# Performance work log

Hardware: AMD Instinct MI355X
Metric: run time of the kernel (lower is better)

Reference implementation:

```python
import jax, jax.numpy as jnp
import numpy as np

H = 256      # hidden_size
NH = 4       # num_heads
HD = H // NH # head_dim
N_NODES = 2048
N_EDGES = 8192
EPS = 1e-5


def _layer_norm(x, g, b):
    mu = jnp.mean(x, axis=-1, keepdims=True)
    var = jnp.mean((x - mu) ** 2, axis=-1, keepdims=True)
    return (x - mu) * jax.lax.rsqrt(var + EPS) * g + b


def setup_inputs() -> dict:
    key = jax.random.key(0)
    ks = jax.random.split(key, 16)
    s = 1.0 / np.sqrt(H)
    inp = {
        "node_features": jax.random.normal(ks[0], (N_NODES, H), jnp.float32),
        "edge_features": jax.random.normal(ks[1], (N_EDGES, H), jnp.float32),
        "in_proj_w": jax.random.uniform(ks[2], (3 * H, H), jnp.float32, -s, s),
        "in_proj_b": jnp.zeros((3 * H,), jnp.float32),
        "out_proj_w": jax.random.uniform(ks[3], (H, H), jnp.float32, -s, s),
        "out_proj_b": jnp.zeros((H,), jnp.float32),
        "mlp_w1": jax.random.uniform(ks[4], (H, H), jnp.float32, -s, s),
        "mlp_b1": jnp.zeros((H,), jnp.float32),
        "mlp_w2": jax.random.uniform(ks[5], (H, H), jnp.float32, -s, s),
        "mlp_b2": jnp.zeros((H,), jnp.float32),
        "nu_w": jax.random.uniform(ks[6], (H, H), jnp.float32, -s, s),
        "nu_b": jnp.zeros((H,), jnp.float32),
        "ln1_g": jnp.ones((H,), jnp.float32),
        "ln1_b": jnp.zeros((H,), jnp.float32),
        "ln2_g": jnp.ones((H,), jnp.float32),
        "ln2_b": jnp.zeros((H,), jnp.float32),
        "edge_index": jax.random.randint(ks[7], (2, N_EDGES), 0, N_NODES, jnp.int32),
    }
    return inp


def reference(node_features, edge_features, in_proj_w, in_proj_b, out_proj_w, out_proj_b,
              mlp_w1, mlp_b1, mlp_w2, mlp_b2, nu_w, nu_b,
              ln1_g, ln1_b, ln2_g, ln2_b, edge_index):
    x = edge_features  # [E, H]; torch MHA with batch=1, seq=E
    qkv = x @ in_proj_w.T + in_proj_b            # [E, 3H]
    q, k, v = jnp.split(qkv, 3, axis=-1)
    q = q.reshape(N_EDGES, NH, HD)
    k = k.reshape(N_EDGES, NH, HD)
    v = v.reshape(N_EDGES, NH, HD)
    scores = jnp.einsum('qhd,khd->hqk', q, k) / np.sqrt(HD)  # [NH, E, E]
    attn = jax.nn.softmax(scores, axis=-1)
    ctx = jnp.einsum('hqk,khd->qhd', attn, v).reshape(N_EDGES, H)
    attended = ctx @ out_proj_w.T + out_proj_b

    e = _layer_norm(edge_features + attended, ln1_g, ln1_b)
    mlp = jax.nn.relu(e @ mlp_w1.T + mlp_b1) @ mlp_w2.T + mlp_b2
    e = _layer_norm(e + mlp, ln2_g, ln2_b)

    dst = edge_index[1]
    seg_sum = jax.ops.segment_sum(e, dst, num_segments=N_NODES)           # [N, H]
    cnt = jax.ops.segment_sum(jnp.ones((N_EDGES,), e.dtype), dst, num_segments=N_NODES)
    node_updates = seg_sum / jnp.maximum(cnt, 1.0)[:, None]               # scatter_mean
    n = node_features + jax.nn.relu(node_updates @ nu_w.T + nu_b)
    return (n, e)
```

## Files before the change

kernel.cpp:

```cpp
#include <hip/hip_runtime.h>

typedef __bf16 bf16_t;
typedef __bf16 bf16x8 __attribute__((ext_vector_type(8)));
typedef __bf16 bf16x4 __attribute__((ext_vector_type(4)));
typedef unsigned short u16x8 __attribute__((ext_vector_type(8)));
typedef unsigned int u32x4 __attribute__((ext_vector_type(4)));
typedef float f32x4 __attribute__((ext_vector_type(4)));
typedef float f32x16 __attribute__((ext_vector_type(16)));
typedef int i32x2 __attribute__((ext_vector_type(2)));

#define NE 8192
#define NN 2048
#define HH 256
#define NSPLIT 8
#define QSCALE 0.18033688011112042f

#if __has_builtin(__builtin_amdgcn_exp2f)
#define EXP2(x) __builtin_amdgcn_exp2f(x)
#else
#define EXP2(x) exp2f(x)
#endif

__device__ inline f32x4 mfma16(bf16x8 a, bf16x8 b, f32x4 c) {
    return __builtin_amdgcn_mfma_f32_16x16x32_bf16(a, b, c, 0, 0, 0);
}
__device__ inline f32x16 mfma32(bf16x8 a, bf16x8 b, f32x16 c) {
    return __builtin_amdgcn_mfma_f32_32x32x16_bf16(a, b, c, 0, 0, 0);
}
__device__ inline unsigned cvtpk(float lo, float hi) {
    unsigned r;
    asm("v_cvt_pk_bf16_f32 %0, %1, %2" : "=v"(r) : "v"(lo), "v"(hi));
    return r;
}

__device__ inline bf16x4 cvt4(float4 v) {
    bf16x4 o;
    o[0] = (bf16_t)v.x; o[1] = (bf16_t)v.y; o[2] = (bf16_t)v.z; o[3] = (bf16_t)v.w;
    return o;
}

__global__ __launch_bounds__(256)
void convert_kernel(const float* __restrict__ ef, const float* __restrict__ wq,
                    const float* __restrict__ wo, const float* __restrict__ w1,
                    const float* __restrict__ w2, const float* __restrict__ wn,
                    bf16_t* __restrict__ ebf, bf16_t* __restrict__ bwq,
                    bf16_t* __restrict__ bwo, bf16_t* __restrict__ bw1,
                    bf16_t* __restrict__ bw2, bf16_t* __restrict__ bwn) {
    int i = blockIdx.x * 256 + threadIdx.x;
    ((bf16x4*)ebf)[i] = cvt4(((const float4*)ef)[i]);
    if (i < 49152) ((bf16x4*)bwq)[i] = cvt4(((const float4*)wq)[i]);
    if (i < 16384) {
        ((bf16x4*)bwo)[i] = cvt4(((const float4*)wo)[i]);
        ((bf16x4*)bw1)[i] = cvt4(((const float4*)w1)[i]);
        ((bf16x4*)bw2)[i] = cvt4(((const float4*)w2)[i]);
        ((bf16x4*)bwn)[i] = cvt4(((const float4*)wn)[i]);
    }
}

template<int ACT, int OUTKIND, int QSC = 0>
__global__ __launch_bounds__(256)
void gemm_kernel(const bf16_t* __restrict__ A, const bf16_t* __restrict__ B,
                 const float* __restrict__ bias, void* __restrict__ out,
                 const float* __restrict__ resid, int M, int N, int K) {
    __shared__ bf16_t As[64][72];
    __shared__ bf16_t Bs[64][72];
    int tid = threadIdx.x;
    int w = tid >> 6, l = tid & 63, hi = l >> 4, c15 = l & 15;
    int wr = w >> 1, wc = w & 1;
    int brow = blockIdx.x * 64, bcol = blockIdx.y * 64;
    int r = tid >> 2, s = tid & 3;

    f32x4 acc[2][2] = {};

    for (int k0 = 0; k0 < K; k0 += 64) {
        __syncthreads();
        bf16x8 a0 = *(const bf16x8*)&A[(long)(brow + r) * K + k0 + s * 16];
        bf16x8 a1 = *(const bf16x8*)&A[(long)(brow + r) * K + k0 + s * 16 + 8];
        bf16x8 b0 = *(const bf16x8*)&B[(long)(bcol + r) * K + k0 + s * 16];
        bf16x8 b1 = *(const bf16x8*)&B[(long)(bcol + r) * K + k0 + s * 16 + 8];
        *(bf16x8*)&As[r][s * 16]     = a0;
        *(bf16x8*)&As[r][s * 16 + 8] = a1;
        *(bf16x8*)&Bs[r][s * 16]     = b0;
        *(bf16x8*)&Bs[r][s * 16 + 8] = b1;
        __syncthreads();
#pragma unroll
        for (int c = 0; c < 2; ++c) {
            bf16x8 af0 = *(const bf16x8*)&As[wr * 32 + c15][c * 32 + hi * 8];
            bf16x8 af1 = *(const bf16x8*)&As[wr * 32 + 16 + c15][c * 32 + hi * 8];
            bf16x8 bf0 = *(const bf16x8*)&Bs[wc * 32 + c15][c * 32 + hi * 8];
            bf16x8 bf1 = *(const bf16x8*)&Bs[wc * 32 + 16 + c15][c * 32 + hi * 8];
            acc[0][0] = mfma16(af0, bf0, acc[0][0]);
            acc[0][1] = mfma16(af0, bf1, acc[0][1]);
            acc[1][0] = mfma16(af1, bf0, acc[1][0]);
            acc[1][1] = mfma16(af1, bf1, acc[1][1]);
        }
    }

    float sc = (QSC && bcol < 256) ? QSCALE : 1.0f;
#pragma unroll
    for (int i = 0; i < 2; ++i)
#pragma unroll
        for (int j = 0; j < 2; ++j)
#pragma unroll
            for (int rg = 0; rg < 4; ++rg) {
                int row = brow + wr * 32 + i * 16 + hi * 4 + rg;
                int col = bcol + wc * 32 + j * 16 + c15;
                float v = (acc[i][j][rg] + bias[col]) * sc;
                if (ACT) v = fmaxf(v, 0.0f);
                if (OUTKIND == 0) {
                    ((float*)out)[(long)row * N + col] = v;
                } else if (OUTKIND == 1) {
                    ((bf16_t*)out)[(long)row * N + col] = (bf16_t)v;
                } else {
                    ((float*)out)[(long)row * N + col] =
                        resid[(long)row * N + col] + fmaxf(v, 0.0f);
                }
            }
}

__global__ __launch_bounds__(256, 2)
void attn_kernel(const bf16_t* __restrict__ qkv, bf16_t* __restrict__ Opart,
                 float* __restrict__ lpart) {
    __shared__ char smem[36864];
    bf16_t (*Ks)[64][72] = (bf16_t (*)[64][72])smem;
    bf16_t (*Vt)[64][72] = (bf16_t (*)[64][72])(smem + 18432);

    int h = blockIdx.x & 3, qb = blockIdx.x >> 2, sp = blockIdx.y;
    int q0 = qb * 256;
    int tid = threadIdx.x;
    int wv = tid >> 6, l = tid & 63, l31 = l & 31, h8 = l >> 5;

    bf16x8 qf[2][4];
#pragma unroll
    for (int qt = 0; qt < 2; ++qt)
#pragma unroll
        for (int dc = 0; dc < 4; ++dc)
            qf[qt][dc] = *(const bf16x8*)&qkv[
                (size_t)(q0 + wv * 64 + qt * 32 + l31) * 768 + h * 64 + dc * 16 + h8 * 8];

    f32x16 o[2][2];
#pragma unroll
    for (int a = 0; a < 2; ++a)
#pragma unroll
        for (int b = 0; b < 2; ++b)
#pragma unroll
            for (int r = 0; r < 16; ++r) o[a][b][r] = 0.f;
    float ls[2] = {0.f, 0.f};

    int kr = tid >> 2, ksc = tid & 3;
    int vp = tid & 31, vc = tid >> 5;
    int kv0 = sp * (NE / NSPLIT);
    const int NT = (NE / NSPLIT) / 64;

    bf16x8 kst0, kst1, vst0, vst1;
    {
        const bf16_t* ksrc = &qkv[(size_t)(kv0 + kr) * 768 + 256 + h * 64 + ksc * 16];
        kst0 = *(const bf16x8*)ksrc; kst1 = *(const bf16x8*)(ksrc + 8);
        const bf16_t* vsrc = &qkv[(size_t)(kv0 + 2 * vp) * 768 + 512 + h * 64 + vc * 8];
        vst0 = *(const bf16x8*)vsrc; vst1 = *(const bf16x8*)(vsrc + 768);
    }
    {
        *(bf16x8*)&Ks[0][kr][ksc * 16]     = kst0;
        *(bf16x8*)&Ks[0][kr][ksc * 16 + 8] = kst1;
        u16x8 ua = __builtin_bit_cast(u16x8, vst0), ub = __builtin_bit_cast(u16x8, vst1);
#pragma unroll
        for (int j = 0; j < 8; ++j) {
            unsigned wd = (unsigned)ua[j] | ((unsigned)ub[j] << 16);
            *(unsigned*)&Vt[0][vc * 8 + j][2 * vp] = wd;
        }
    }

    for (int t = 0; t < NT; ++t) {
        int cur = t & 1;
        __syncthreads();
        if (t + 1 < NT) {
            int kt = kv0 + (t + 1) * 64;
            const bf16_t* ksrc = &qkv[(size_t)(kt + kr) * 768 + 256 + h * 64 + ksc * 16];
            kst0 = *(const bf16x8*)ksrc; kst1 = *(const bf16x8*)(ksrc + 8);
            const bf16_t* vsrc = &qkv[(size_t)(kt + 2 * vp) * 768 + 512 + h * 64 + vc * 8];
            vst0 = *(const bf16x8*)vsrc; vst1 = *(const bf16x8*)(vsrc + 768);
        }

#pragma unroll
        for (int kvt = 0; kvt < 2; ++kvt) {
            bf16x8 kf[4];
#pragma unroll
            for (int dc = 0; dc < 4; ++dc)
                kf[dc] = *(const bf16x8*)&Ks[cur][kvt * 32 + l31][dc * 16 + h8 * 8];
            f32x16 s[2];
#pragma unroll
            for (int qt = 0; qt < 2; ++qt) {
#pragma unroll
                for (int r = 0; r < 16; ++r) s[qt][r] = 0.f;
#pragma unroll
                for (int dc = 0; dc < 4; ++dc)
                    s[qt] = mfma32(kf[dc], qf[qt][dc], s[qt]);
            }
            bf16x8 bfr[2][2];
#pragma unroll
            for (int qt = 0; qt < 2; ++qt) {
                float p[16];
#pragma unroll
                for (int r = 0; r < 16; ++r) { p[r] = EXP2(s[qt][r]); ls[qt] += p[r]; }
#pragma unroll
                for (int half = 0; half < 2; ++half) {
                    i32x2 r0 = __builtin_amdgcn_permlane32_swap(
                        (int)cvtpk(p[8 * half + 0], p[8 * half + 1]),
                        (int)cvtpk(p[8 * half + 4], p[8 * half + 5]), false, false);
                    i32x2 r1 = __builtin_amdgcn_permlane32_swap(
                        (int)cvtpk(p[8 * half + 2], p[8 * half + 3]),
                        (int)cvtpk(p[8 * half + 6], p[8 * half + 7]), false, false);
                    u32x4 wds;
                    wds[0] = (unsigned)r0[0]; wds[1] = (unsigned)r1[0];
                    wds[2] = (unsigned)r0[1]; wds[3] = (unsigned)r1[1];
                    bfr[qt][half] = __builtin_bit_cast(bf16x8, wds);
                }
            }
#pragma unroll
            for (int dt = 0; dt < 2; ++dt) {
                bf16x8 vf[2];
#pragma unroll
                for (int half = 0; half < 2; ++half)
                    vf[half] = *(const bf16x8*)&Vt[cur][dt * 32 + l31][(kvt * 2 + half) * 16 + h8 * 8];
#pragma unroll
                for (int qt = 0; qt < 2; ++qt)
#pragma unroll
                    for (int half = 0; half < 2; ++half)
                        o[dt][qt] = mfma32(vf[half], bfr[qt][half], o[dt][qt]);
            }
        }

        if (t + 1 < NT) {
            int nb = (t + 1) & 1;
            *(bf16x8*)&Ks[nb][kr][ksc * 16]     = kst0;
            *(bf16x8*)&Ks[nb][kr][ksc * 16 + 8] = kst1;
            u16x8 ua = __builtin_bit_cast(u16x8, vst0), ub = __builtin_bit_cast(u16x8, vst1);
#pragma unroll
            for (int j = 0; j < 8; ++j) {
                unsigned wd = (unsigned)ua[j] | ((unsigned)ub[j] << 16);
                *(unsigned*)&Vt[nb][vc * 8 + j][2 * vp] = wd;
            }
        }
    }

#pragma unroll
    for (int qt = 0; qt < 2; ++qt) {
        float lt = ls[qt] + __shfl_xor(ls[qt], 32);
        if (l < 32)
            lpart[((size_t)sp * 4 + h) * NE + q0 + wv * 64 + qt * 32 + l31] = lt;
    }

    float* Of = (float*)smem;
#pragma unroll
    for (int pass = 0; pass < 2; ++pass) {
        __syncthreads();
        if ((wv >> 1) == pass) {
#pragma unroll
            for (int dt = 0; dt < 2; ++dt)
#pragma unroll
                for (int qt = 0; qt < 2; ++qt)
#pragma unroll
                    for (int r = 0; r < 16; ++r) {
                        int qrel = (wv & 1) * 64 + qt * 32 + l31;
                        int d = dt * 32 + (r & 3) + 8 * (r >> 2) + 4 * h8;
                        Of[qrel * 68 + d] = o[dt][qt][r];
                    }
        }
        __syncthreads();
        {
            int rr = tid >> 1, hf = tid & 1;
            bf16_t* dst = &Opart[(size_t)sp * NE * 256 +
                                 (size_t)(q0 + pass * 128 + rr) * 256 + h * 64 + hf * 32];
#pragma unroll
            for (int i = 0; i < 4; ++i) {
                float4 va = *(float4*)&Of[rr * 68 + hf * 32 + i * 8];
                float4 vb = *(float4*)&Of[rr * 68 + hf * 32 + i * 8 + 4];
                bf16x8 ob;
                ob[0] = (bf16_t)va.x; ob[1] = (bf16_t)va.y;
                ob[2] = (bf16_t)va.z; ob[3] = (bf16_t)va.w;
                ob[4] = (bf16_t)vb.x; ob[5] = (bf16_t)vb.y;
                ob[6] = (bf16_t)vb.z; ob[7] = (bf16_t)vb.w;
                *(bf16x8*)&dst[i * 8] = ob;
            }
        }
    }
}

__global__ __launch_bounds__(256)
void attn_merge_kernel(const bf16_t* __restrict__ Opart, const float* __restrict__ lpart,
                       bf16_t* __restrict__ ctx) {
    int i = blockIdx.x * 256 + threadIdx.x;
    int q = i >> 5;
    int h = (i & 31) >> 3;
    float sum[8] = {};
    float lsum = 0.f;
#pragma unroll
    for (int sp = 0; sp < NSPLIT; ++sp) {
        bf16x8 v = ((const bf16x8*)Opart)[(size_t)sp * (NE * 32) + i];
#pragma unroll
        for (int j = 0; j < 8; ++j) sum[j] += (float)v[j];
        lsum += lpart[((size_t)sp * 4 + h) * NE + q];
    }
    float rl = 1.0f / lsum;
    bf16x8 c;
#pragma unroll
    for (int j = 0; j < 8; ++j) c[j] = (bf16_t)(sum[j] * rl);
    ((bf16x8*)ctx)[i] = c;
}

__global__ __launch_bounds__(256)
void ln_kernel(const float* __restrict__ x, const float* __restrict__ y,
               const float* __restrict__ g, const float* __restrict__ b,
               float* __restrict__ outf, bf16_t* __restrict__ outb) {
    int row = blockIdx.x * 4 + (threadIdx.x >> 6);
    int l = threadIdx.x & 63;
    float4 v = ((const float4*)&x[(long)row * 256])[l];
    float4 uu = ((const float4*)&y[(long)row * 256])[l];
    float a0 = v.x + uu.x, a1 = v.y + uu.y, a2 = v.z + uu.z, a3 = v.w + uu.w;

    float s = a0 + a1 + a2 + a3;
#pragma unroll
    for (int off = 1; off < 64; off <<= 1) s += __shfl_xor(s, off);
    float mu = s * (1.0f / 256.0f);

    float d0 = a0 - mu, d1 = a1 - mu, d2 = a2 - mu, d3 = a3 - mu;
    float q = d0 * d0 + d1 * d1 + d2 * d2 + d3 * d3;
#pragma unroll
    for (int off = 1; off < 64; off <<= 1) q += __shfl_xor(q, off);
    float rs = rsqrtf(q * (1.0f / 256.0f) + 1e-5f);

    float4 gg = ((const float4*)g)[l];
    float4 bb = ((const float4*)b)[l];
    float o0 = d0 * rs * gg.x + bb.x;
    float o1 = d1 * rs * gg.y + bb.y;
    float o2 = d2 * rs * gg.z + bb.z;
    float o3 = d3 * rs * gg.w + bb.w;
    float4 ov; ov.x = o0; ov.y = o1; ov.z = o2; ov.w = o3;
    ((float4*)&outf[(long)row * 256])[l] = ov;
    if (outb) {
        bf16x4 ob;
        ob[0] = (bf16_t)o0; ob[1] = (bf16_t)o1; ob[2] = (bf16_t)o2; ob[3] = (bf16_t)o3;
        ((bf16x4*)&outb[(long)row * 256])[l] = ob;
    }
}

__global__ __launch_bounds__(256)
void scatter_kernel(const float* __restrict__ e, const int* __restrict__ ei,
                    float* __restrict__ acc, float* __restrict__ cnt) {
    int edge = blockIdx.x;
    int dst = ei[NE + edge];
    int t = threadIdx.x;
    atomicAdd(&acc[(long)dst * 256 + t], e[(long)edge * 256 + t]);
    if (t == 0) atomicAdd(&cnt[dst], 1.0f);
}

__global__ __launch_bounds__(256)
void upd_kernel(const float* __restrict__ acc, const float* __restrict__ cnt,
                bf16_t* __restrict__ ub) {
    int i = blockIdx.x * 256 + threadIdx.x;
    int row = i >> 8;
    ub[i] = (bf16_t)(acc[i] / fmaxf(cnt[row], 1.0f));
}

extern "C" void kernel_launch(void* const* d_in, const int* in_sizes, int n_in,
                              void* d_out, int out_size, void* d_ws, size_t ws_size,
                              hipStream_t stream) {
    const float* node_features = (const float*)d_in[0];
    const float* edge_features = (const float*)d_in[1];
    const float* in_proj_w  = (const float*)d_in[2];
    const float* in_proj_b  = (const float*)d_in[3];
    const float* out_proj_w = (const float*)d_in[4];
    const float* out_proj_b = (const float*)d_in[5];
    const float* mlp_w1 = (const float*)d_in[6];
    const float* mlp_b1 = (const float*)d_in[7];
    const float* mlp_w2 = (const float*)d_in[8];
    const float* mlp_b2 = (const float*)d_in[9];
    const float* nu_w   = (const float*)d_in[10];
    const float* nu_b   = (const float*)d_in[11];
    const float* ln1_g  = (const float*)d_in[12];
    const float* ln1_b  = (const float*)d_in[13];
    const float* ln2_g  = (const float*)d_in[14];
    const float* ln2_b  = (const float*)d_in[15];
    const int*   edge_index = (const int*)d_in[16];

    char* ws = (char*)d_ws;
    size_t off = 0;
    auto alloc = [&](size_t bytes) {
        char* p = ws + off;
        off = (off + bytes + 255) & ~(size_t)255;
        return p;
    };
    bf16_t* ebf   = (bf16_t*)alloc(NE * HH * 2);
    bf16_t* bwq   = (bf16_t*)alloc(768 * 256 * 2);
    bf16_t* bwo   = (bf16_t*)alloc(256 * 256 * 2);
    bf16_t* bw1   = (bf16_t*)alloc(256 * 256 * 2);
    bf16_t* bw2   = (bf16_t*)alloc(256 * 256 * 2);
    bf16_t* bwn   = (bf16_t*)alloc(256 * 256 * 2);
    bf16_t* qkv   = (bf16_t*)alloc((size_t)NE * 768 * 2);
    bf16_t* ctx   = (bf16_t*)alloc((size_t)NE * HH * 2);
    float*  lpart = (float*)alloc((size_t)NSPLIT * 4 * NE * 4);
    float*  acc   = (float*)alloc((size_t)(NN * HH + NN) * 4);
    float*  cnt   = acc + (size_t)NN * HH;
    bf16_t* updb  = (bf16_t*)alloc((size_t)NN * HH * 2);
    size_t offB = off;
    bf16_t* Opart = (bf16_t*)alloc((size_t)NSPLIT * NE * HH * 2);
    off = offB;
    float*  attended = (float*)alloc((size_t)NE * HH * 4);
    float*  e1f   = (float*)alloc((size_t)NE * HH * 4);
    bf16_t* e1b   = (bf16_t*)alloc((size_t)NE * HH * 2);
    bf16_t* hbuf  = (bf16_t*)alloc((size_t)NE * HH * 2);
    float*  mlpout = (float*)alloc((size_t)NE * HH * 4);

    float* nout = (float*)d_out;
    float* eout = (float*)d_out + (size_t)NN * HH;

    convert_kernel<<<2048, 256, 0, stream>>>(edge_features, in_proj_w, out_proj_w,
                                             mlp_w1, mlp_w2, nu_w,
                                             ebf, bwq, bwo, bw1, bw2, bwn);

    gemm_kernel<0, 1, 1><<<dim3(NE / 64, 768 / 64), 256, 0, stream>>>(
        ebf, bwq, in_proj_b, qkv, nullptr, NE, 768, 256);

    attn_kernel<<<dim3(128, NSPLIT), 256, 0, stream>>>(qkv, Opart, lpart);
    attn_merge_kernel<<<1024, 256, 0, stream>>>(Opart, lpart, ctx);

    gemm_kernel<0, 0><<<dim3(NE / 64, 256 / 64), 256, 0, stream>>>(
        ctx, bwo, out_proj_b, attended, nullptr, NE, 256, 256);

    ln_kernel<<<NE / 4, 256, 0, stream>>>(edge_features, attended, ln1_g, ln1_b,
                                          e1f, e1b);

    gemm_kernel<1, 1><<<dim3(NE / 64, 256 / 64), 256, 0, stream>>>(
        e1b, bw1, mlp_b1, hbuf, nullptr, NE, 256, 256);

    gemm_kernel<0, 0><<<dim3(NE / 64, 256 / 64), 256, 0, stream>>>(
        hbuf, bw2, mlp_b2, mlpout, nullptr, NE, 256, 256);

    ln_kernel<<<NE / 4, 256, 0, stream>>>(e1f, mlpout, ln2_g, ln2_b,
                                          eout, (bf16_t*)nullptr);

    hipMemsetAsync(acc, 0, (size_t)(NN * HH + NN) * 4, stream);
    scatter_kernel<<<NE, 256, 0, stream>>>(eout, edge_index, acc, cnt);
    upd_kernel<<<NN * HH / 256, 256, 0, stream>>>(acc, cnt, updb);

    gemm_kernel<0, 2><<<dim3(NN / 64, 256 / 64), 256, 0, stream>>>(
        updb, bwn, nu_b, nout, node_features, NN, 256, 256);
}
```

Measured before the change: 146.6 us.

## Fuse fp32-to-bf16 conversion into GEMM loads and LayerNorm into GEMM epilogues

Removes the separate conversion kernel so the GEMMs read fp32 inputs and weights directly and convert to bf16 while staging into shared memory. Adds a full-row GEMM kernel (64x256 tile) that applies bias, residual add and LayerNorm in its epilogue, replacing the out-proj, MLP2 and both standalone LayerNorm kernels. This drops the fp32 intermediate buffers and two launches. It also adds s_setprio around the MFMA blocks in attention. The trade-offs are that weights are reconverted in every block and the fused LN kernel runs only 128 blocks, which may underfill the GPU.

```diff
diff --git a/kernel.cpp b/kernel.cpp
--- a/kernel.cpp
+++ b/kernel.cpp
@@ -32,34 +32,16 @@
     asm("v_cvt_pk_bf16_f32 %0, %1, %2" : "=v"(r) : "v"(lo), "v"(hi));
     return r;
 }
-
-__device__ inline bf16x4 cvt4(float4 v) {
-    bf16x4 o;
-    o[0] = (bf16_t)v.x; o[1] = (bf16_t)v.y; o[2] = (bf16_t)v.z; o[3] = (bf16_t)v.w;
+__device__ inline bf16x8 cvt8(float4 a, float4 b) {
+    bf16x8 o;
+    o[0] = (bf16_t)a.x; o[1] = (bf16_t)a.y; o[2] = (bf16_t)a.z; o[3] = (bf16_t)a.w;
+    o[4] = (bf16_t)b.x; o[5] = (bf16_t)b.y; o[6] = (bf16_t)b.z; o[7] = (bf16_t)b.w;
     return o;
 }
 
+template<int ACT, int OUTKIND, int QSC, int AF32, int BF32>
 __global__ __launch_bounds__(256)
-void convert_kernel(const float* __restrict__ ef, const float* __restrict__ wq,
-                    const float* __restrict__ wo, const float* __restrict__ w1,
-                    const float* __restrict__ w2, const float* __restrict__ wn,
-                    bf16_t* __restrict__ ebf, bf16_t* __restrict__ bwq,
-                    bf16_t* __restrict__ bwo, bf16_t* __restrict__ bw1,
-                    bf16_t* __restrict__ bw2, bf16_t* __restrict__ bwn) {
-    int i = blockIdx.x * 256 + threadIdx.x;
-    ((bf16x4*)ebf)[i] = cvt4(((const float4*)ef)[i]);
-    if (i < 49152) ((bf16x4*)bwq)[i] = cvt4(((const float4*)wq)[i]);
-    if (i < 16384) {
-        ((bf16x4*)bwo)[i] = cvt4(((const float4*)wo)[i]);
-        ((bf16x4*)bw1)[i] = cvt4(((const float4*)w1)[i]);
-        ((bf16x4*)bw2)[i] = cvt4(((const float4*)w2)[i]);
-        ((bf16x4*)bwn)[i] = cvt4(((const float4*)wn)[i]);
-    }
-}
-
-template<int ACT, int OUTKIND, int QSC = 0>
-__global__ __launch_bounds__(256)
-void gemm_kernel(const bf16_t* __restrict__ A, const bf16_t* __restrict__ B,
+void gemm_kernel(const void* __restrict__ Av, const void* __restrict__ Bv,
                  const float* __restrict__ bias, void* __restrict__ out,
                  const float* __restrict__ resid, int M, int N, int K) {
     __shared__ bf16_t As[64][72];
@@ -74,14 +56,30 @@
 
     for (int k0 = 0; k0 < K; k0 += 64) {
         __syncthreads();
-        bf16x8 a0 = *(const bf16x8*)&A[(long)(brow + r) * K + k0 + s * 16];
-        bf16x8 a1 = *(const bf16x8*)&A[(long)(brow + r) * K + k0 + s * 16 + 8];
-        bf16x8 b0 = *(const bf16x8*)&B[(long)(bcol + r) * K + k0 + s * 16];
-        bf16x8 b1 = *(const bf16x8*)&B[(long)(bcol + r) * K + k0 + s * 16 + 8];
-        *(bf16x8*)&As[r][s * 16]     = a0;
-        *(bf16x8*)&As[r][s * 16 + 8] = a1;
-        *(bf16x8*)&Bs[r][s * 16]     = b0;
-        *(bf16x8*)&Bs[r][s * 16 + 8] = b1;
+        if (AF32) {
+            const float* Af = (const float*)Av;
+            const float* p = &Af[(long)(brow + r) * K + k0 + s * 16];
+            float4 f0 = *(const float4*)p,       f1 = *(const float4*)(p + 4);
+            float4 f2 = *(const float4*)(p + 8), f3 = *(const float4*)(p + 12);
+            *(bf16x8*)&As[r][s * 16]     = cvt8(f0, f1);
+            *(bf16x8*)&As[r][s * 16 + 8] = cvt8(f2, f3);
+        } else {
+            const bf16_t* Ab = (const bf16_t*)Av;
+            *(bf16x8*)&As[r][s * 16]     = *(const bf16x8*)&Ab[(long)(brow + r) * K + k0 + s * 16];
+            *(bf16x8*)&As[r][s * 16 + 8] = *(const bf16x8*)&Ab[(long)(brow + r) * K + k0 + s * 16 + 8];
+        }
+        if (BF32) {
+            const float* Bf = (const float*)Bv;
+            const float* p = &Bf[(long)(bcol + r) * K + k0 + s * 16];
+            float4 f0 = *(const float4*)p,       f1 = *(const float4*)(p + 4);
+            float4 f2 = *(const float4*)(p + 8), f3 = *(const float4*)(p + 12);
+            *(bf16x8*)&Bs[r][s * 16]     = cvt8(f0, f1);
+            *(bf16x8*)&Bs[r][s * 16 + 8] = cvt8(f2, f3);
+        } else {
+            const bf16_t* Bb = (const bf16_t*)Bv;
+            *(bf16x8*)&Bs[r][s * 16]     = *(const bf16x8*)&Bb[(long)(bcol + r) * K + k0 + s * 16];
+            *(bf16x8*)&Bs[r][s * 16 + 8] = *(const bf16x8*)&Bb[(long)(bcol + r) * K + k0 + s * 16 + 8];
+        }
         __syncthreads();
 #pragma unroll
         for (int c = 0; c < 2; ++c) {
@@ -118,6 +116,80 @@
             }
 }
 
+template<int WRITE_BF16>
+__global__ __launch_bounds__(256)
+void gemm_ln_kernel(const bf16_t* __restrict__ A, const float* __restrict__ Bw,
+                    const float* __restrict__ bias, const float* __restrict__ resid,
+                    const float* __restrict__ g, const float* __restrict__ bv,
+                    float* __restrict__ outf, bf16_t* __restrict__ outb) {
+    __shared__ bf16_t As[64][72];
+    __shared__ bf16_t Bs[256][72];
+    int tid = threadIdx.x;
+    int w = tid >> 6, l = tid & 63, hi = l >> 4, c15 = l & 15;
+    int brow = blockIdx.x * 64;
+    int r = tid >> 2, s = tid & 3;
+
+    f32x4 acc[16] = {};
+
+    for (int k0 = 0; k0 < 256; k0 += 64) {
+        __syncthreads();
+        *(bf16x8*)&As[r][s * 16]     = *(const bf16x8*)&A[(long)(brow + r) * 256 + k0 + s * 16];
+        *(bf16x8*)&As[r][s * 16 + 8] = *(const bf16x8*)&A[(long)(brow + r) * 256 + k0 + s * 16 + 8];
+        const float* bp = &Bw[(long)tid * 256 + k0];
+#pragma unroll
+        for (int c = 0; c < 8; ++c) {
+            float4 fa = *(const float4*)&bp[c * 8];
+            float4 fb = *(const float4*)&bp[c * 8 + 4];
+            *(bf16x8*)&Bs[tid][c * 8] = cvt8(fa, fb);
+        }
+        __syncthreads();
+#pragma unroll
+        for (int ks = 0; ks < 2; ++ks) {
+            bf16x8 af = *(const bf16x8*)&As[w * 16 + c15][ks * 32 + hi * 8];
+#pragma unroll
+            for (int j = 0; j < 16; ++j) {
+                bf16x8 bfr = *(const bf16x8*)&Bs[j * 16 + c15][ks * 32 + hi * 8];
+                acc[j] = mfma16(af, bfr, acc[j]);
+            }
+        }
+    }
+
+    float gs[16], bs[16];
+#pragma unroll
+    for (int j = 0; j < 16; ++j) {
+        int col = j * 16 + c15;
+        float bb = bias[col];
+#pragma unroll
+        for (int rg = 0; rg < 4; ++rg) acc[j][rg] += bb;
+        gs[j] = g[col]; bs[j] = bv[col];
+    }
+#pragma unroll
+    for (int rg = 0; rg < 4; ++rg) {
+        int row = brow + w * 16 + hi * 4 + rg;
+        float v[16];
+        float sm = 0.f, qs = 0.f;
+#pragma unroll
+        for (int j = 0; j < 16; ++j) {
+            v[j] = acc[j][rg] + resid[(long)row * 256 + j * 16 + c15];
+            sm += v[j]; qs += v[j] * v[j];
+        }
+#pragma unroll
+        for (int m = 1; m < 16; m <<= 1) {
+            sm += __shfl_xor(sm, m);
+            qs += __shfl_xor(qs, m);
+        }
+        float mu = sm * (1.f / 256.f);
+        float var = qs * (1.f / 256.f) - mu * mu;
+        float rs = rsqrtf(var + 1e-5f);
+#pragma unroll
+        for (int j = 0; j < 16; ++j) {
+            float o = (v[j] - mu) * rs * gs[j] + bs[j];
+            outf[(long)row * 256 + j * 16 + c15] = o;
+            if (WRITE_BF16) outb[(long)row * 256 + j * 16 + c15] = (bf16_t)o;
+        }
+    }
+}
+
 __global__ __launch_bounds__(256, 2)
 void attn_kernel(const bf16_t* __restrict__ qkv, bf16_t* __restrict__ Opart,
                  float* __restrict__ lpart) {
@@ -188,6 +260,7 @@
             for (int dc = 0; dc < 4; ++dc)
                 kf[dc] = *(const bf16x8*)&Ks[cur][kvt * 32 + l31][dc * 16 + h8 * 8];
             f32x16 s[2];
+            __builtin_amdgcn_s_setprio(1);
 #pragma unroll
             for (int qt = 0; qt < 2; ++qt) {
 #pragma unroll
@@ -196,6 +269,7 @@
                 for (int dc = 0; dc < 4; ++dc)
                     s[qt] = mfma32(kf[dc], qf[qt][dc], s[qt]);
             }
+            __builtin_amdgcn_s_setprio(0);
             bf16x8 bfr[2][2];
 #pragma unroll
             for (int qt = 0; qt < 2; ++qt) {
@@ -216,6 +290,7 @@
                     bfr[qt][half] = __builtin_bit_cast(bf16x8, wds);
                 }
             }
+            __builtin_amdgcn_s_setprio(1);
 #pragma unroll
             for (int dt = 0; dt < 2; ++dt) {
                 bf16x8 vf[2];
@@ -228,6 +303,7 @@
                     for (int half = 0; half < 2; ++half)
                         o[dt][qt] = mfma32(vf[half], bfr[qt][half], o[dt][qt]);
             }
+            __builtin_amdgcn_s_setprio(0);
         }
 
         if (t + 1 < NT) {
@@ -306,42 +382,6 @@
 #pragma unroll
     for (int j = 0; j < 8; ++j) c[j] = (bf16_t)(sum[j] * rl);
     ((bf16x8*)ctx)[i] = c;
-}
-
-__global__ __launch_bounds__(256)
-void ln_kernel(const float* __restrict__ x, const float* __restrict__ y,
-               const float* __restrict__ g, const float* __restrict__ b,
-               float* __restrict__ outf, bf16_t* __restrict__ outb) {
-    int row = blockIdx.x * 4 + (threadIdx.x >> 6);
-    int l = threadIdx.x & 63;
-    float4 v = ((const float4*)&x[(long)row * 256])[l];
-    float4 uu = ((const float4*)&y[(long)row * 256])[l];
-    float a0 = v.x + uu.x, a1 = v.y + uu.y, a2 = v.z + uu.z, a3 = v.w + uu.w;
-
-    float s = a0 + a1 + a2 + a3;
-#pragma unroll
-    for (int off = 1; off < 64; off <<= 1) s += __shfl_xor(s, off);
-    float mu = s * (1.0f / 256.0f);
-
-    float d0 = a0 - mu, d1 = a1 - mu, d2 = a2 - mu, d3 = a3 - mu;
-    float q = d0 * d0 + d1 * d1 + d2 * d2 + d3 * d3;
-#pragma unroll
-    for (int off = 1; off < 64; off <<= 1) q += __shfl_xor(q, off);
-    float rs = rsqrtf(q * (1.0f / 256.0f) + 1e-5f);
-
-    float4 gg = ((const float4*)g)[l];
-    float4 bb = ((const float4*)b)[l];
-    float o0 = d0 * rs * gg.x + bb.x;
-    float o1 = d1 * rs * gg.y + bb.y;
-    float o2 = d2 * rs * gg.z + bb.z;
-    float o3 = d3 * rs * gg.w + bb.w;
-    float4 ov; ov.x = o0; ov.y = o1; ov.z = o2; ov.w = o3;
-    ((float4*)&outf[(long)row * 256])[l] = ov;
-    if (outb) {
-        bf16x4 ob;
-        ob[0] = (bf16_t)o0; ob[1] = (bf16_t)o1; ob[2] = (bf16_t)o2; ob[3] = (bf16_t)o3;
-        ((bf16x4*)&outb[(long)row * 256])[l] = ob;
-    }
 }
 
 __global__ __launch_bounds__(256)
@@ -390,12 +430,6 @@
         off = (off + bytes + 255) & ~(size_t)255;
         return p;
     };
-    bf16_t* ebf   = (bf16_t*)alloc(NE * HH * 2);
-    bf16_t* bwq   = (bf16_t*)alloc(768 * 256 * 2);
-    bf16_t* bwo   = (bf16_t*)alloc(256 * 256 * 2);
-    bf16_t* bw1   = (bf16_t*)alloc(256 * 256 * 2);
-    bf16_t* bw2   = (bf16_t*)alloc(256 * 256 * 2);
-    bf16_t* bwn   = (bf16_t*)alloc(256 * 256 * 2);
     bf16_t* qkv   = (bf16_t*)alloc((size_t)NE * 768 * 2);
     bf16_t* ctx   = (bf16_t*)alloc((size_t)NE * HH * 2);
     float*  lpart = (float*)alloc((size_t)NSPLIT * 4 * NE * 4);
@@ -405,44 +439,32 @@
     size_t offB = off;
     bf16_t* Opart = (bf16_t*)alloc((size_t)NSPLIT * NE * HH * 2);
     off = offB;
-    float*  attended = (float*)alloc((size_t)NE * HH * 4);
     float*  e1f   = (float*)alloc((size_t)NE * HH * 4);
     bf16_t* e1b   = (bf16_t*)alloc((size_t)NE * HH * 2);
     bf16_t* hbuf  = (bf16_t*)alloc((size_t)NE * HH * 2);
-    float*  mlpout = (float*)alloc((size_t)NE * HH * 4);
 
     float* nout = (float*)d_out;
     float* eout = (float*)d_out + (size_t)NN * HH;
 
-    convert_kernel<<<2048, 256, 0, stream>>>(edge_features, in_proj_w, out_proj_w,
-                                             mlp_w1, mlp_w2, nu_w,
-                                             ebf, bwq, bwo, bw1, bw2, bwn);
-
-    gemm_kernel<0, 1, 1><<<dim3(NE / 64, 768 / 64), 256, 0, stream>>>(
-        ebf, bwq, in_proj_b, qkv, nullptr, NE, 768, 256);
+    gemm_kernel<0, 1, 1, 1, 1><<<dim3(NE / 64, 768 / 64), 256, 0, stream>>>(
+        edge_features, in_proj_w, in_proj_b, qkv, nullptr, NE, 768, 256);
 
     attn_kernel<<<dim3(128, NSPLIT), 256, 0, stream>>>(qkv, Opart, lpart);
     attn_merge_kernel<<<1024, 256, 0, stream>>>(Opart, lpart, ctx);
 
-    gemm_kernel<0, 0><<<dim3(NE / 64, 256 / 64), 256, 0, stream>>>(
-        ctx, bwo, out_proj_b, attended, nullptr, NE, 256, 256);
-
-    ln_kernel<<<NE / 4, 256, 0, stream>>>(edge_features, attended, ln1_g, ln1_b,
-                                          e1f, e1b);
-
-    gemm_kernel<1, 1><<<dim3(NE / 64, 256 / 64), 256, 0, stream>>>(
-        e1b, bw1, mlp_b1, hbuf, nullptr, NE, 256, 256);
-
-    gemm_kernel<0, 0><<<dim3(NE / 64, 256 / 64), 256, 0, stream>>>(
-        hbuf, bw2, mlp_b2, mlpout, nullptr, NE, 256, 256);
-
-    ln_kernel<<<NE / 4, 256, 0, stream>>>(e1f, mlpout, ln2_g, ln2_b,
-                                          eout, (bf16_t*)nullptr);
+    gemm_ln_kernel<1><<<NE / 64, 256, 0, stream>>>(
+        ctx, out_proj_w, out_proj_b, edge_features, ln1_g, ln1_b, e1f, e1b);
+
+    gemm_kernel<1, 1, 0, 0, 1><<<dim3(NE / 64, 256 / 64), 256, 0, stream>>>(
+        e1b, mlp_w1, mlp_b1, hbuf, nullptr, NE, 256, 256);
+
+    gemm_ln_kernel<0><<<NE / 64, 256, 0, stream>>>(
+        hbuf, mlp_w2, mlp_b2, e1f, ln2_g, ln2_b, eout, nullptr);
 
     hipMemsetAsync(acc, 0, (size_t)(NN * HH + NN) * 4, stream);
     scatter_kernel<<<NE, 256, 0, stream>>>(eout, edge_index, acc, cnt);
     upd_kernel<<<NN * HH / 256, 256, 0, stream>>>(acc, cnt, updb);
 
-    gemm_kernel<0, 2><<<dim3(NN / 64, 256 / 64), 256, 0, stream>>>(
-        updb, bwn, nu_b, nout, node_features, NN, 256, 256);
-}
+    gemm_kernel<0, 2, 0, 0, 1><<<dim3(NN / 64, 256 / 64), 256, 0, stream>>>(
+        updb, nu_w, nu_b, nout, node_features, NN, 256, 256);
+}
```

Result: slower. 167.5 us (+14.2%).
